# Kernel optimization log

Hardware: AMD Instinct MI355X
Metric: run time of the kernel (lower is better)

The kernel has to match this reference:

```python
import jax, jax.numpy as jnp
import numpy as np

NUM_CLASSES = 80
NMS_THRESH = 0.5      # cfg.MODEL.ROI_HEADS.NMS_THRESH_TEST
SCORE_THRESH = 0.5    # cfg.MODEL.ROI_HEADS.SCORE_THRESH_TEST
IMG_H, IMG_W = 800.0, 1333.0  # clip bounds (image_size)


def _pairwise_iou(boxes):
    # boxes: [N,4] xyxy -> IoU [N,N]
    x1, y1, x2, y2 = boxes[:, 0], boxes[:, 1], boxes[:, 2], boxes[:, 3]
    area = jnp.maximum(x2 - x1, 0.0) * jnp.maximum(y2 - y1, 0.0)
    xx1 = jnp.maximum(x1[:, None], x1[None, :])
    yy1 = jnp.maximum(y1[:, None], y1[None, :])
    xx2 = jnp.minimum(x2[:, None], x2[None, :])
    yy2 = jnp.minimum(y2[:, None], y2[None, :])
    inter = jnp.maximum(xx2 - xx1, 0.0) * jnp.maximum(yy2 - yy1, 0.0)
    union = area[:, None] + area[None, :] - inter
    return inter / jnp.maximum(union, 1e-9)


def _nms_mask(boxes, scores, thresh):
    # torchvision-style greedy NMS; returns boolean keep mask in original order
    N = boxes.shape[0]
    order = jnp.argsort(-scores)
    iou = _pairwise_iou(boxes[order])  # [N,N] in score-descending order
    idx = jnp.arange(N)

    def body(i, keep):
        # if box i survives, suppress all lower-scored boxes with IoU > thresh
        sup = (iou[i] > thresh) & keep[i] & (idx > i)
        return keep & ~sup

    keep = jax.lax.fori_loop(0, N, body, jnp.ones(N, dtype=bool))
    return jnp.zeros(N, dtype=bool).at[order].set(keep)


def setup_inputs() -> dict:
    key = jax.random.key(0)
    k1, k2, k3, k4 = jax.random.split(key, 4)
    B, N = 8, 512
    # realistic xyxy boxes inside the image
    xy = jax.random.uniform(k1, (B, N, NUM_CLASSES, 2)) * jnp.array([IMG_W, IMG_H])
    wh = jax.random.uniform(k2, (B, N, NUM_CLASSES, 2)) * 200.0 + 4.0
    boxes = jnp.concatenate([xy, xy + wh], axis=-1).astype(jnp.float32)
    score_logits = (jax.random.normal(k3, (B, N, NUM_CLASSES + 1)) * 2.0).astype(jnp.float32)
    scale = jax.random.uniform(k4, (B, 2), minval=0.5, maxval=1.5).astype(jnp.float32)
    return {"boxes": boxes, "score_logits": score_logits, "scale": scale}


def reference(boxes, score_logits, scale):
    # --- get_output_boxes: scale + clip ---
    probs = jax.nn.softmax(score_logits, axis=-1)  # [B,N,81] (predict_probs)
    s4 = jnp.stack([scale[:, 0], scale[:, 1], scale[:, 0], scale[:, 1]], axis=-1)  # [B,4]
    scaled = boxes * s4[:, None, None, :]
    hi = jnp.array([IMG_W, IMG_H, IMG_W, IMG_H], dtype=boxes.dtype)
    clipped = jnp.clip(scaled, 0.0, hi)  # [B,N,80,4]

    # --- select_boxes: per-class NMS (class-parallel instead of python loop) ---
    cls_boxes = jnp.moveaxis(clipped, 2, 1)           # [B,80,N,4]
    cls_scores = jnp.moveaxis(probs[..., 1:], 2, 1)   # [B,80,N] (skip background col 0)
    nms = jax.vmap(jax.vmap(lambda b, s: _nms_mask(b, s, NMS_THRESH)))
    keep_mask = nms(cls_boxes, cls_scores)            # [B,80,N]

    # cumulative max_conf update over classes == elementwise max over kept scores
    max_conf = jnp.max(jnp.where(keep_mask, cls_scores, 0.0), axis=1)  # [B,N]
    keep = (max_conf >= SCORE_THRESH).astype(jnp.float32)              # [B,N]
    return max_conf, keep
```

## Files before the change

kernel.cpp:

```cpp
#include <hip/hip_runtime.h>
#include <cstdint>

#define NB 8
#define NN 512
#define NC 80
#define NCL 81
#define NMS_TH 0.5f
#define SCORE_TH 0.5f
#define IMGW 1333.0f
#define IMGH 800.0f
#define CUT 0.018f

__device__ __forceinline__ uint64_t shfl_xor64(uint64_t x, int m) {
    uint32_t lo = __shfl_xor((uint32_t)(x & 0xffffffffull), m, 64);
    uint32_t hi = __shfl_xor((uint32_t)(x >> 32), m, 64);
    return ((uint64_t)hi << 32) | lo;
}
__device__ __forceinline__ float bcastf(float v, int l) {
    return __uint_as_float((uint32_t)__builtin_amdgcn_readlane((int)__float_as_uint(v), l));
}
__device__ __forceinline__ uint64_t readlane64(uint64_t v, int l) {
    uint32_t lo = (uint32_t)__builtin_amdgcn_readlane((int)(uint32_t)(v & 0xffffffffull), l);
    uint32_t hi = (uint32_t)__builtin_amdgcn_readlane((int)(uint32_t)(v >> 32), l);
    return ((uint64_t)hi << 32) | lo;
}

__global__ __launch_bounds__(256) void k_probs(const float* __restrict__ logits,
                                               float* __restrict__ probsT,
                                               float* __restrict__ maxconf,
                                               float* __restrict__ keepout) {
    __shared__ float lp[16][81];
    const int wv = threadIdx.x >> 6, lane = threadIdx.x & 63;
    const int row0 = blockIdx.x * 16;
    const int b = row0 >> 9, n0 = row0 & (NN - 1);

    for (int r = 0; r < 4; ++r) {
        const int rl = wv * 4 + r;
        const int row = row0 + rl;
        const float* p = logits + (size_t)row * NCL;
        float v0 = p[lane];
        bool has1 = (lane + 64) < NCL;
        float v1 = has1 ? p[lane + 64] : -INFINITY;
        float m = fmaxf(v0, v1);
#pragma unroll
        for (int off = 32; off; off >>= 1) m = fmaxf(m, __shfl_xor(m, off));
        float e0 = expf(v0 - m);
        float e1 = has1 ? expf(v1 - m) : 0.0f;
        float s = e0 + e1;
#pragma unroll
        for (int off = 32; off; off >>= 1) s += __shfl_xor(s, off);
        if (lane >= 1)  lp[rl][lane - 1]  = e0 / s;
        if (has1)       lp[rl][lane + 63] = e1 / s;
    }
    if (threadIdx.x < 16)                       maxconf[row0 + threadIdx.x] = 0.0f;
    else if (threadIdx.x < 32)                  keepout[row0 + (threadIdx.x - 16)] = 0.0f;
    __syncthreads();

    for (int it = 0; it < 5; ++it) {
        const int idx = it * 256 + threadIdx.x;
        const int c = idx >> 4, nl = idx & 15;
        probsT[(size_t)(b * NC + c) * NN + n0 + nl] = lp[nl][c];
    }
}

__global__ __launch_bounds__(64) void k_softmax_stats(const float* __restrict__ logits,
                                                      float* __restrict__ stats,
                                                      float* __restrict__ maxconf,
                                                      float* __restrict__ keepout) {
    int row = blockIdx.x;
    int lane = threadIdx.x;
    const float* p = logits + (size_t)row * NCL;
    float v0 = p[lane];
    bool has1 = (lane + 64) < NCL;
    float v1 = has1 ? p[lane + 64] : -INFINITY;
    float m = fmaxf(v0, v1);
#pragma unroll
    for (int off = 32; off; off >>= 1) m = fmaxf(m, __shfl_xor(m, off));
    float s = expf(v0 - m) + (has1 ? expf(v1 - m) : 0.0f);
#pragma unroll
    for (int off = 32; off; off >>= 1) s += __shfl_xor(s, off);
    if (lane == 0) { stats[2 * row] = m; stats[2 * row + 1] = s; }
    if (lane == 1) maxconf[row] = 0.0f;
    if (lane == 2) keepout[row] = 0.0f;
}

__device__ __forceinline__ void nms64(const uint64_t k0, const int M, const int lane,
                                      const float* __restrict__ boxBase,
                                      const float sx, const float sy, const int obase,
                                      float* __restrict__ maxconf,
                                      float* __restrict__ keepout) {
    float x1 = 0.f, y1 = 0.f, x2 = 0.f, y2 = 0.f, ar = 0.f;
    int nidx = 0;
    if (lane < M) {
        nidx = NN - 1 - (int)(uint32_t)(k0 & 0xffffffffull);
        const float4 bp = *reinterpret_cast<const float4*>(boxBase + (size_t)nidx * (NC * 4));
        x1 = fminf(fmaxf(bp.x * sx, 0.f), IMGW);
        y1 = fminf(fmaxf(bp.y * sy, 0.f), IMGH);
        x2 = fminf(fmaxf(bp.z * sx, 0.f), IMGW);
        y2 = fminf(fmaxf(bp.w * sy, 0.f), IMGH);
        ar = fmaxf(x2 - x1, 0.f) * fmaxf(y2 - y1, 0.f);
    }

    uint64_t pmv = 0;
    int rankv = lane;
    const int M2 = M & ~1;
    for (int ii = 0; ii < M2; ii += 2) {
        const uint64_t kA = readlane64(k0, ii);
        const uint64_t kB = readlane64(k0, ii + 1);
        const float aX1 = bcastf(x1, ii),     aY1 = bcastf(y1, ii);
        const float aX2 = bcastf(x2, ii),     aY2 = bcastf(y2, ii);
        const float aAr = bcastf(ar, ii);
        const float bX1 = bcastf(x1, ii + 1), bY1 = bcastf(y1, ii + 1);
        const float bX2 = bcastf(x2, ii + 1), bY2 = bcastf(y2, ii + 1);
        const float bAr = bcastf(ar, ii + 1);
        float dxA = fminf(aX2, x2) - fmaxf(aX1, x1);
        float dyA = fminf(aY2, y2) - fmaxf(aY1, y1);
        float dxB = fminf(bX2, x2) - fmaxf(bX1, x1);
        float dyB = fminf(bY2, y2) - fmaxf(bY1, y1);
        float inA = fmaxf(dxA, 0.f) * fmaxf(dyA, 0.f);
        float inB = fmaxf(dxB, 0.f) * fmaxf(dyB, 0.f);
        const uint64_t hibA = __ballot(k0 > kA);
        const uint64_t hibB = __ballot(k0 > kB);
        const uint64_t ioA = __ballot(inA > NMS_TH * fmaxf(aAr + ar - inA, 1e-9f));
        const uint64_t ioB = __ballot(inB > NMS_TH * fmaxf(bAr + ar - inB, 1e-9f));
        if (lane == ii)     { pmv = ioA & ~(1ull << ii);       rankv = (int)__popcll(hibA); }
        if (lane == ii + 1) { pmv = ioB & ~(1ull << (ii + 1)); rankv = (int)__popcll(hibB); }
    }
    if (M & 1) {
        const int ii = M - 1;
        const uint64_t kA = readlane64(k0, ii);
        const float aX1 = bcastf(x1, ii), aY1 = bcastf(y1, ii);
        const float aX2 = bcastf(x2, ii), aY2 = bcastf(y2, ii);
        const float aAr = bcastf(ar, ii);
        float dxA = fminf(aX2, x2) - fmaxf(aX1, x1);
        float dyA = fminf(aY2, y2) - fmaxf(aY1, y1);
        float inA = fmaxf(dxA, 0.f) * fmaxf(dyA, 0.f);
        const uint64_t hibA = __ballot(k0 > kA);
        const uint64_t ioA = __ballot(inA > NMS_TH * fmaxf(aAr + ar - inA, 1e-9f));
        if (lane == ii) { pmv = ioA & ~(1ull << ii); rankv = (int)__popcll(hibA); }
    }

    const int permv = __builtin_amdgcn_ds_permute(rankv << 2, lane);

    uint64_t rw = 0, kb = 0;
    int sNext = __builtin_amdgcn_readlane(permv, 0);
    for (int t = 0; t < M; ++t) {
        const int s = sNext;
        sNext = __builtin_amdgcn_readlane(permv, (t + 1 < M) ? (t + 1) : t);
        if (!((rw >> s) & 1ull)) {
            kb |= (1ull << s);
            rw |= readlane64(pmv, s);
        }
    }

    if (lane < M && ((kb >> lane) & 1ull)) {
        const uint32_t sb = (uint32_t)(k0 >> 32);
        atomicMax((int*)maxconf + obase + nidx, (int)sb);
        if (sb >= 0x3F000000u)
            keepout[obase + nidx] = 1.0f;
    }
}

template<int NS>
__device__ __forceinline__ void sort_desc(uint64_t (&key)[NS], const int lane) {
#pragma unroll
    for (int k = 2; k <= NS * 64; k <<= 1) {
#pragma unroll
        for (int j = k >> 1; j > 0; j >>= 1) {
            if (j >= 64) {
                const int m = j >> 6;
#pragma unroll
                for (int s = 0; s < NS; ++s) {
                    if ((s & m) == 0) {
                        const int sp = s | m;
                        const bool up = (((s << 6) & k) != 0);
                        uint64_t a = key[s], bb = key[sp];
                        bool altb = a < bb;
                        uint64_t mn = altb ? a : bb, mx = altb ? bb : a;
                        key[s]  = up ? mn : mx;
                        key[sp] = up ? mx : mn;
                    }
                }
            } else {
#pragma unroll
                for (int s = 0; s < NS; ++s) {
                    uint64_t a = key[s];
                    uint64_t bb = shfl_xor64(a, j);
                    const int v = (s << 6) | lane;
                    bool up = ((v & k) != 0);
                    bool lower = ((lane & j) == 0);
                    bool altb = a < bb;
                    uint64_t mn = altb ? a : bb, mx = altb ? bb : a;
                    key[s] = (lower == up) ? mn : mx;
                }
            }
        }
    }
}

template<int NS>
__device__ __forceinline__ void nms_core(uint64_t (&key)[NS], const int M, const int lane,
                                         const float* __restrict__ boxBase,
                                         const float sx, const float sy, const int obase,
                                         float* __restrict__ maxconf,
                                         float* __restrict__ keepout) {
    float rx1[NS], ry1[NS], rx2[NS], ry2[NS], ra[NS];
    int sidx[NS];
#pragma unroll
    for (int s = 0; s < NS; ++s) {
        rx1[s] = ry1[s] = rx2[s] = ry2[s] = ra[s] = 0.f;
        sidx[s] = 0;
        const int r = (s << 6) | lane;
        if (r < M) {
            const int n = NN - 1 - (int)(uint32_t)(key[s] & 0xffffffffull);
            sidx[s] = n;
            const float4 bp = *reinterpret_cast<const float4*>(boxBase + (size_t)n * (NC * 4));
            float x1 = fminf(fmaxf(bp.x * sx, 0.f), IMGW);
            float y1 = fminf(fmaxf(bp.y * sy, 0.f), IMGH);
            float x2 = fminf(fmaxf(bp.z * sx, 0.f), IMGW);
            float y2 = fminf(fmaxf(bp.w * sy, 0.f), IMGH);
            rx1[s] = x1; ry1[s] = y1; rx2[s] = x2; ry2[s] = y2;
            ra[s] = fmaxf(x2 - x1, 0.f) * fmaxf(y2 - y1, 0.f);
        }
    }

    uint64_t pm[NS][NS];
#pragma unroll
    for (int s = 0; s < NS; ++s)
#pragma unroll
        for (int w = 0; w < NS; ++w) pm[s][w] = 0;
#pragma unroll
    for (int s = 0; s < NS; ++s) {
        if ((s << 6) < M) {
            const int hi = min(64, M - (s << 6));
            const int hi2 = hi & ~1;
            for (int ii = 0; ii < hi2; ii += 2) {
                const float aX1 = bcastf(rx1[s], ii),     aY1 = bcastf(ry1[s], ii);
                const float aX2 = bcastf(rx2[s], ii),     aY2 = bcastf(ry2[s], ii);
                const float aAr = bcastf(ra[s],  ii);
                const float bX1 = bcastf(rx1[s], ii + 1), bY1 = bcastf(ry1[s], ii + 1);
                const float bX2 = bcastf(rx2[s], ii + 1), bY2 = bcastf(ry2[s], ii + 1);
                const float bAr = bcastf(ra[s],  ii + 1);
#pragma unroll
                for (int w = s; w < NS; ++w) {
                    if ((w << 6) < M) {
                        float dxA = fminf(aX2, rx2[w]) - fmaxf(aX1, rx1[w]);
                        float dyA = fminf(aY2, ry2[w]) - fmaxf(aY1, ry1[w]);
                        float dxB = fminf(bX2, rx2[w]) - fmaxf(bX1, rx1[w]);
                        float dyB = fminf(bY2, ry2[w]) - fmaxf(bY1, ry1[w]);
                        float inA = fmaxf(dxA, 0.f) * fmaxf(dyA, 0.f);
                        float inB = fmaxf(dxB, 0.f) * fmaxf(dyB, 0.f);
                        uint64_t bmA = __ballot(inA > NMS_TH * fmaxf(aAr + ra[w] - inA, 1e-9f));
                        uint64_t bmB = __ballot(inB > NMS_TH * fmaxf(bAr + ra[w] - inB, 1e-9f));
                        if (w == s) { bmA &= ~(1ull << ii); bmB &= ~(1ull << (ii + 1)); }
                        if (lane == ii)     pm[s][w] = bmA;
                        if (lane == ii + 1) pm[s][w] = bmB;
                    }
                }
            }
            if (hi & 1) {
                const int ii = hi - 1;
                const float aX1 = bcastf(rx1[s], ii), aY1 = bcastf(ry1[s], ii);
                const float aX2 = bcastf(rx2[s], ii), aY2 = bcastf(ry2[s], ii);
                const float aAr = bcastf(ra[s],  ii);
#pragma unroll
                for (int w = s; w < NS; ++w) {
                    if ((w << 6) < M) {
                        float dxA = fminf(aX2, rx2[w]) - fmaxf(aX1, rx1[w]);
                        float dyA = fminf(aY2, ry2[w]) - fmaxf(aY1, ry1[w]);
                        float inA = fmaxf(dxA, 0.f) * fmaxf(dyA, 0.f);
                        uint64_t bmA = __ballot(inA > NMS_TH * fmaxf(aAr + ra[w] - inA, 1e-9f));
                        if (w == s) bmA &= ~(1ull << ii);
                        if (lane == ii) pm[s][w] = bmA;
                    }
                }
            }
        }
    }

    uint64_t rw[NS], kb[NS];
#pragma unroll
    for (int s = 0; s < NS; ++s) { rw[s] = 0; kb[s] = 0; }
#pragma unroll
    for (int s = 0; s < NS; ++s) {
        if ((s << 6) < M) {
            const int Ms = M - (s << 6);
            const uint64_t valid = (Ms >= 64) ? ~0ull : ((1ull << Ms) - 1ull);
            uint64_t cand = valid & ~rw[s];
            while (cand) {
                const int l = __builtin_ctzll(cand);
                kb[s] |= (1ull << l);
#pragma unroll
                for (int w = s; w < NS; ++w)
                    if ((w << 6) < M) rw[w] |= readlane64(pm[s][w], l);
                cand = valid & ~rw[s] & ((~0ull << l) << 1);
            }
        }
    }

#pragma unroll
    for (int s = 0; s < NS; ++s) {
        const int r = (s << 6) | lane;
        if (r < M && ((kb[s] >> lane) & 1ull)) {
            const uint32_t sb = (uint32_t)(key[s] >> 32);
            atomicMax((int*)maxconf + obase + sidx[s], (int)sb);
            if (sb >= 0x3F000000u)
                keepout[obase + sidx[s]] = 1.0f;
        }
    }
}

__global__ __launch_bounds__(256) void k_nms(const float* __restrict__ boxes,
                                             const float* __restrict__ probsT,
                                             const float* __restrict__ logits,
                                             const float* __restrict__ scale,
                                             const float* __restrict__ stats,
                                             float* __restrict__ maxconf,
                                             float* __restrict__ keepout) {
    const int wv = threadIdx.x >> 6;
    const int lane = threadIdx.x & 63;
    const int prob = blockIdx.x * 4 + wv;
    const int b = prob / NC, c = prob % NC;

    __shared__ uint64_t lk[4][NN];

    uint64_t key8[8];
    int M = 0;
    if (probsT) {
        const float* pp = probsT + (size_t)(b * NC + c) * NN;
#pragma unroll
        for (int s = 0; s < 8; ++s) {
            const int n = (s << 6) | lane;
            const float p = pp[n];
            const bool pass = (p >= CUT);
            key8[s] = pass ? (((uint64_t)__float_as_uint(p) << 32) | (uint32_t)(NN - 1 - n)) : 0ull;
            M += (int)__popcll(__ballot(pass));
        }
    } else {
        const float2* st2 = (const float2*)stats;
#pragma unroll
        for (int s = 0; s < 8; ++s) {
            const int n = (s << 6) | lane;
            const int row = b * NN + n;
            float2 ms = st2[row];
            const float p = expf(logits[(size_t)row * NCL + (c + 1)] - ms.x) / ms.y;
            const bool pass = (p >= CUT);
            key8[s] = pass ? (((uint64_t)__float_as_uint(p) << 32) | (uint32_t)(NN - 1 - n)) : 0ull;
            M += (int)__popcll(__ballot(pass));
        }
    }
    if (M == 0) return;

    int cb = 0;
#pragma unroll
    for (int s = 0; s < 8; ++s) {
        const uint64_t bm = __ballot(key8[s] != 0ull);
        const int rank = cb + (int)__popcll(bm & ((1ull << lane) - 1ull));
        if (key8[s]) lk[wv][rank] = key8[s];
        cb += (int)__popcll(bm);
    }

    const float sx = scale[2 * b], sy = scale[2 * b + 1];
    const float* boxBase = boxes + (size_t)(b * NN * NC + c) * 4;
    const int obase = b * NN;

    if (M <= 64) {
        const uint64_t k0 = (lane < M) ? lk[wv][lane] : 0ull;
        nms64(k0, M, lane, boxBase, sx, sy, obase, maxconf, keepout);
    } else if (M <= 128) {
        uint64_t kk[2];
#pragma unroll
        for (int s = 0; s < 2; ++s) { const int r = (s << 6) | lane; kk[s] = (r < M) ? lk[wv][r] : 0ull; }
        sort_desc<2>(kk, lane);
        nms_core<2>(kk, M, lane, boxBase, sx, sy, obase, maxconf, keepout);
    } else if (M <= 256) {
        uint64_t kk[4];
#pragma unroll
        for (int s = 0; s < 4; ++s) { const int r = (s << 6) | lane; kk[s] = (r < M) ? lk[wv][r] : 0ull; }
        sort_desc<4>(kk, lane);
        nms_core<4>(kk, M, lane, boxBase, sx, sy, obase, maxconf, keepout);
    } else {
        uint64_t kk[8];
#pragma unroll
        for (int s = 0; s < 8; ++s) { const int r = (s << 6) | lane; kk[s] = (r < M) ? lk[wv][r] : 0ull; }
        sort_desc<8>(kk, lane);
        nms_core<8>(kk, M, lane, boxBase, sx, sy, obase, maxconf, keepout);
    }
}

extern "C" void kernel_launch(void* const* d_in, const int* in_sizes, int n_in,
                              void* d_out, int out_size, void* d_ws, size_t ws_size,
                              hipStream_t stream) {
    const float* boxes  = (const float*)d_in[0];
    const float* logits = (const float*)d_in[1];
    const float* scale  = (const float*)d_in[2];
    float* out  = (float*)d_out;
    float* keep = out + NB * NN;

    const size_t needWs = (size_t)NB * NN * NC * sizeof(float);
    if (ws_size >= needWs) {
        float* probsT = (float*)d_ws;
        hipLaunchKernelGGL(k_probs, dim3(NB * NN / 16), dim3(256), 0, stream,
                           logits, probsT, out, keep);
        hipLaunchKernelGGL(k_nms, dim3(NB * NC / 4), dim3(256), 0, stream,
                           boxes, probsT, logits, scale, (const float*)nullptr, out, keep);
    } else {
        float* stats = (float*)d_ws;
        hipLaunchKernelGGL(k_softmax_stats, dim3(NB * NN), dim3(64), 0, stream,
                           logits, stats, out, keep);
        hipLaunchKernelGGL(k_nms, dim3(NB * NC / 4), dim3(256), 0, stream,
                           boxes, (const float*)nullptr, logits, scale, stats, out, keep);
    }
}
```

Before: 28.03 us.

## Fuse softmax-transpose and NMS into one cooperative kernel with grid sync

Merges the probability/transpose kernel and the per-class NMS kernel into a single cooperative launch of 256 blocks, separated by a grid-wide barrier. Each block first computes softmax for its rows into shared memory and writes the transposed probabilities, then after the barrier its waves run NMS for their class problems, reusing the same shared buffer. This removes one kernel launch and the gap between the two kernels, at the cost of a grid sync and requiring all blocks to be co-resident. If the cooperative launch fails, it falls back to the two-kernel path.

Measured after the change: 83.77 us. 199% more time.

```diff
diff --git a/kernel.cpp b/kernel.cpp
--- a/kernel.cpp
+++ b/kernel.cpp
@@ -1,5 +1,8 @@
 #include <hip/hip_runtime.h>
+#include <hip/hip_cooperative_groups.h>
 #include <cstdint>
+
+namespace cg = cooperative_groups;
 
 #define NB 8
 #define NN 512
@@ -25,13 +28,13 @@
     return ((uint64_t)hi << 32) | lo;
 }
 
-__global__ __launch_bounds__(256) void k_probs(const float* __restrict__ logits,
-                                               float* __restrict__ probsT,
-                                               float* __restrict__ maxconf,
-                                               float* __restrict__ keepout) {
-    __shared__ float lp[16][81];
+__device__ __forceinline__ void probs16_body(const float* __restrict__ logits,
+                                             float* __restrict__ probsT,
+                                             float* __restrict__ maxconf,
+                                             float* __restrict__ keepout,
+                                             const int blk, float (*lp)[81]) {
     const int wv = threadIdx.x >> 6, lane = threadIdx.x & 63;
-    const int row0 = blockIdx.x * 16;
+    const int row0 = blk * 16;
     const int b = row0 >> 9, n0 = row0 & (NN - 1);
 
     for (int r = 0; r < 4; ++r) {
@@ -52,8 +55,8 @@
         if (lane >= 1)  lp[rl][lane - 1]  = e0 / s;
         if (has1)       lp[rl][lane + 63] = e1 / s;
     }
-    if (threadIdx.x < 16)                       maxconf[row0 + threadIdx.x] = 0.0f;
-    else if (threadIdx.x < 32)                  keepout[row0 + (threadIdx.x - 16)] = 0.0f;
+    if (threadIdx.x < 16)      maxconf[row0 + threadIdx.x] = 0.0f;
+    else if (threadIdx.x < 32) keepout[row0 + (threadIdx.x - 16)] = 0.0f;
     __syncthreads();
 
     for (int it = 0; it < 5; ++it) {
@@ -61,27 +64,6 @@
         const int c = idx >> 4, nl = idx & 15;
         probsT[(size_t)(b * NC + c) * NN + n0 + nl] = lp[nl][c];
     }
-}
-
-__global__ __launch_bounds__(64) void k_softmax_stats(const float* __restrict__ logits,
-                                                      float* __restrict__ stats,
-                                                      float* __restrict__ maxconf,
-                                                      float* __restrict__ keepout) {
-    int row = blockIdx.x;
-    int lane = threadIdx.x;
-    const float* p = logits + (size_t)row * NCL;
-    float v0 = p[lane];
-    bool has1 = (lane + 64) < NCL;
-    float v1 = has1 ? p[lane + 64] : -INFINITY;
-    float m = fmaxf(v0, v1);
-#pragma unroll
-    for (int off = 32; off; off >>= 1) m = fmaxf(m, __shfl_xor(m, off));
-    float s = expf(v0 - m) + (has1 ? expf(v1 - m) : 0.0f);
-#pragma unroll
-    for (int off = 32; off; off >>= 1) s += __shfl_xor(s, off);
-    if (lane == 0) { stats[2 * row] = m; stats[2 * row + 1] = s; }
-    if (lane == 1) maxconf[row] = 0.0f;
-    if (lane == 2) keepout[row] = 0.0f;
 }
 
 __device__ __forceinline__ void nms64(const uint64_t k0, const int M, const int lane,
@@ -310,19 +292,16 @@
     }
 }
 
-__global__ __launch_bounds__(256) void k_nms(const float* __restrict__ boxes,
-                                             const float* __restrict__ probsT,
-                                             const float* __restrict__ logits,
-                                             const float* __restrict__ scale,
-                                             const float* __restrict__ stats,
-                                             float* __restrict__ maxconf,
-                                             float* __restrict__ keepout) {
-    const int wv = threadIdx.x >> 6;
-    const int lane = threadIdx.x & 63;
-    const int prob = blockIdx.x * 4 + wv;
+__device__ __forceinline__ void nms_wave(const float* __restrict__ boxes,
+                                         const float* __restrict__ probsT,
+                                         const float* __restrict__ logits,
+                                         const float* __restrict__ scale,
+                                         const float* __restrict__ stats,
+                                         float* __restrict__ maxconf,
+                                         float* __restrict__ keepout,
+                                         const int prob, const int lane,
+                                         uint64_t* __restrict__ lkw) {
     const int b = prob / NC, c = prob % NC;
-
-    __shared__ uint64_t lk[4][NN];
 
     uint64_t key8[8];
     int M = 0;
@@ -356,7 +335,7 @@
     for (int s = 0; s < 8; ++s) {
         const uint64_t bm = __ballot(key8[s] != 0ull);
         const int rank = cb + (int)__popcll(bm & ((1ull << lane) - 1ull));
-        if (key8[s]) lk[wv][rank] = key8[s];
+        if (key8[s]) lkw[rank] = key8[s];
         cb += (int)__popcll(bm);
     }
 
@@ -365,27 +344,87 @@
     const int obase = b * NN;
 
     if (M <= 64) {
-        const uint64_t k0 = (lane < M) ? lk[wv][lane] : 0ull;
+        const uint64_t k0 = (lane < M) ? lkw[lane] : 0ull;
         nms64(k0, M, lane, boxBase, sx, sy, obase, maxconf, keepout);
     } else if (M <= 128) {
         uint64_t kk[2];
 #pragma unroll
-        for (int s = 0; s < 2; ++s) { const int r = (s << 6) | lane; kk[s] = (r < M) ? lk[wv][r] : 0ull; }
+        for (int s = 0; s < 2; ++s) { const int r = (s << 6) | lane; kk[s] = (r < M) ? lkw[r] : 0ull; }
         sort_desc<2>(kk, lane);
         nms_core<2>(kk, M, lane, boxBase, sx, sy, obase, maxconf, keepout);
     } else if (M <= 256) {
         uint64_t kk[4];
 #pragma unroll
-        for (int s = 0; s < 4; ++s) { const int r = (s << 6) | lane; kk[s] = (r < M) ? lk[wv][r] : 0ull; }
+        for (int s = 0; s < 4; ++s) { const int r = (s << 6) | lane; kk[s] = (r < M) ? lkw[r] : 0ull; }
         sort_desc<4>(kk, lane);
         nms_core<4>(kk, M, lane, boxBase, sx, sy, obase, maxconf, keepout);
     } else {
         uint64_t kk[8];
 #pragma unroll
-        for (int s = 0; s < 8; ++s) { const int r = (s << 6) | lane; kk[s] = (r < M) ? lk[wv][r] : 0ull; }
+        for (int s = 0; s < 8; ++s) { const int r = (s << 6) | lane; kk[s] = (r < M) ? lkw[r] : 0ull; }
         sort_desc<8>(kk, lane);
         nms_core<8>(kk, M, lane, boxBase, sx, sy, obase, maxconf, keepout);
     }
+}
+
+__global__ __launch_bounds__(256) void k_fused(const float* __restrict__ boxes,
+                                               const float* __restrict__ logits,
+                                               const float* __restrict__ scale,
+                                               float* __restrict__ probsT,
+                                               float* __restrict__ maxconf,
+                                               float* __restrict__ keepout) {
+    __shared__ uint64_t lk[4][NN];
+    probs16_body(logits, probsT, maxconf, keepout, blockIdx.x, (float(*)[81])lk);
+    __threadfence();
+    cg::this_grid().sync();
+
+    const int wv = threadIdx.x >> 6, lane = threadIdx.x & 63;
+    const int prob = blockIdx.x * 4 + wv;
+    if (prob >= NB * NC) return;
+    nms_wave(boxes, probsT, nullptr, scale, nullptr, maxconf, keepout, prob, lane, lk[wv]);
+}
+
+__global__ __launch_bounds__(256) void k_probs(const float* __restrict__ logits,
+                                               float* __restrict__ probsT,
+                                               float* __restrict__ maxconf,
+                                               float* __restrict__ keepout) {
+    __shared__ float lp[16][81];
+    probs16_body(logits, probsT, maxconf, keepout, blockIdx.x, lp);
+}
+
+__global__ __launch_bounds__(64) void k_softmax_stats(const float* __restrict__ logits,
+                                                      float* __restrict__ stats,
+                                                      float* __restrict__ maxconf,
+                                                      float* __restrict__ keepout) {
+    int row = blockIdx.x;
+    int lane = threadIdx.x;
+    const float* p = logits + (size_t)row * NCL;
+    float v0 = p[lane];
+    bool has1 = (lane + 64) < NCL;
+    float v1 = has1 ? p[lane + 64] : -INFINITY;
+    float m = fmaxf(v0, v1);
+#pragma unroll
+    for (int off = 32; off; off >>= 1) m = fmaxf(m, __shfl_xor(m, off));
+    float s = expf(v0 - m) + (has1 ? expf(v1 - m) : 0.0f);
+#pragma unroll
+    for (int off = 32; off; off >>= 1) s += __shfl_xor(s, off);
+    if (lane == 0) { stats[2 * row] = m; stats[2 * row + 1] = s; }
+    if (lane == 1) maxconf[row] = 0.0f;
+    if (lane == 2) keepout[row] = 0.0f;
+}
+
+__global__ __launch_bounds__(256) void k_nms(const float* __restrict__ boxes,
+                                             const float* __restrict__ probsT,
+                                             const float* __restrict__ logits,
+                                             const float* __restrict__ scale,
+                                             const float* __restrict__ stats,
+                                             float* __restrict__ maxconf,
+                                             float* __restrict__ keepout) {
+    __shared__ uint64_t lk[4][NN];
+    const int wv = threadIdx.x >> 6, lane = threadIdx.x & 63;
+    const int prob = blockIdx.x * 4 + wv;
+    if (prob >= NB * NC) return;
+    nms_wave(boxes, probsT, logits, scale, stats, maxconf, keepout, prob, lane, lk[wv]);
 }
 
 extern "C" void kernel_launch(void* const* d_in, const int* in_sizes, int n_in,
@@ -400,6 +439,12 @@
     const size_t needWs = (size_t)NB * NN * NC * sizeof(float);
     if (ws_size >= needWs) {
         float* probsT = (float*)d_ws;
+        void* args[] = {(void*)&boxes, (void*)&logits, (void*)&scale,
+                        (void*)&probsT, (void*)&out, (void*)&keep};
+        hipError_t e = hipLaunchCooperativeKernel((const void*)k_fused, dim3(256), dim3(256),
+                                                  args, 0, stream);
+        if (e == hipSuccess) return;
+        (void)hipGetLastError();
         hipLaunchKernelGGL(k_probs, dim3(NB * NN / 16), dim3(256), 0, stream,
                            logits, probsT, out, keep);
         hipLaunchKernelGGL(k_nms, dim3(NB * NC / 4), dim3(256), 0, stream,
```

## Fuse softmax statistics into NMS kernel and drop the probability workspace

Applied to the files above, without the earlier changes.

Merges the separate softmax/probability kernel and the NMS kernel into one launch. Each block recomputes the per-row softmax max and sum for all 512 rows of its batch into shared memory, then builds the per-class probabilities directly from the logits. Output initialisation is replaced by atomicMax with zero, and keep-flag writes become atomicMax, so no ordering between blocks is needed. This removes a kernel launch and the transposed probability buffer round-trip. In exchange, softmax work is repeated across the 20 blocks that share a batch, each thread reads its logits row with uncoalesced strided loads, and outputs are no longer reset to zero.

Measured after the change: 30.53 us. 1.09x slower.

```diff
diff --git a/kernel.cpp b/kernel.cpp
--- a/kernel.cpp
+++ b/kernel.cpp
@@ -23,65 +23,6 @@
     uint32_t lo = (uint32_t)__builtin_amdgcn_readlane((int)(uint32_t)(v & 0xffffffffull), l);
     uint32_t hi = (uint32_t)__builtin_amdgcn_readlane((int)(uint32_t)(v >> 32), l);
     return ((uint64_t)hi << 32) | lo;
-}
-
-__global__ __launch_bounds__(256) void k_probs(const float* __restrict__ logits,
-                                               float* __restrict__ probsT,
-                                               float* __restrict__ maxconf,
-                                               float* __restrict__ keepout) {
-    __shared__ float lp[16][81];
-    const int wv = threadIdx.x >> 6, lane = threadIdx.x & 63;
-    const int row0 = blockIdx.x * 16;
-    const int b = row0 >> 9, n0 = row0 & (NN - 1);
-
-    for (int r = 0; r < 4; ++r) {
-        const int rl = wv * 4 + r;
-        const int row = row0 + rl;
-        const float* p = logits + (size_t)row * NCL;
-        float v0 = p[lane];
-        bool has1 = (lane + 64) < NCL;
-        float v1 = has1 ? p[lane + 64] : -INFINITY;
-        float m = fmaxf(v0, v1);
-#pragma unroll
-        for (int off = 32; off; off >>= 1) m = fmaxf(m, __shfl_xor(m, off));
-        float e0 = expf(v0 - m);
-        float e1 = has1 ? expf(v1 - m) : 0.0f;
-        float s = e0 + e1;
-#pragma unroll
-        for (int off = 32; off; off >>= 1) s += __shfl_xor(s, off);
-        if (lane >= 1)  lp[rl][lane - 1]  = e0 / s;
-        if (has1)       lp[rl][lane + 63] = e1 / s;
-    }
-    if (threadIdx.x < 16)                       maxconf[row0 + threadIdx.x] = 0.0f;
-    else if (threadIdx.x < 32)                  keepout[row0 + (threadIdx.x - 16)] = 0.0f;
-    __syncthreads();
-
-    for (int it = 0; it < 5; ++it) {
-        const int idx = it * 256 + threadIdx.x;
-        const int c = idx >> 4, nl = idx & 15;
-        probsT[(size_t)(b * NC + c) * NN + n0 + nl] = lp[nl][c];
-    }
-}
-
-__global__ __launch_bounds__(64) void k_softmax_stats(const float* __restrict__ logits,
-                                                      float* __restrict__ stats,
-                                                      float* __restrict__ maxconf,
-                                                      float* __restrict__ keepout) {
-    int row = blockIdx.x;
-    int lane = threadIdx.x;
-    const float* p = logits + (size_t)row * NCL;
-    float v0 = p[lane];
-    bool has1 = (lane + 64) < NCL;
-    float v1 = has1 ? p[lane + 64] : -INFINITY;
-    float m = fmaxf(v0, v1);
-#pragma unroll
-    for (int off = 32; off; off >>= 1) m = fmaxf(m, __shfl_xor(m, off));
-    float s = expf(v0 - m) + (has1 ? expf(v1 - m) : 0.0f);
-#pragma unroll
-    for (int off = 32; off; off >>= 1) s += __shfl_xor(s, off);
-    if (lane == 0) { stats[2 * row] = m; stats[2 * row + 1] = s; }
-    if (lane == 1) maxconf[row] = 0.0f;
-    if (lane == 2) keepout[row] = 0.0f;
 }
 
 __device__ __forceinline__ void nms64(const uint64_t k0, const int M, const int lane,
@@ -157,7 +98,7 @@
         const uint32_t sb = (uint32_t)(k0 >> 32);
         atomicMax((int*)maxconf + obase + nidx, (int)sb);
         if (sb >= 0x3F000000u)
-            keepout[obase + nidx] = 1.0f;
+            atomicMax((int*)keepout + obase + nidx, 0x3F800000);
     }
 }
 
@@ -305,49 +246,68 @@
             const uint32_t sb = (uint32_t)(key[s] >> 32);
             atomicMax((int*)maxconf + obase + sidx[s], (int)sb);
             if (sb >= 0x3F000000u)
-                keepout[obase + sidx[s]] = 1.0f;
-        }
-    }
-}
-
-__global__ __launch_bounds__(256) void k_nms(const float* __restrict__ boxes,
-                                             const float* __restrict__ probsT,
+                atomicMax((int*)keepout + obase + sidx[s], 0x3F800000);
+        }
+    }
+}
+
+__global__ __launch_bounds__(256) void k_all(const float* __restrict__ boxes,
                                              const float* __restrict__ logits,
                                              const float* __restrict__ scale,
-                                             const float* __restrict__ stats,
                                              float* __restrict__ maxconf,
                                              float* __restrict__ keepout) {
-    const int wv = threadIdx.x >> 6;
-    const int lane = threadIdx.x & 63;
-    const int prob = blockIdx.x * 4 + wv;
-    const int b = prob / NC, c = prob % NC;
-
+    __shared__ float smM[NN], smS[NN];
     __shared__ uint64_t lk[4][NN];
+
+    const int wv = threadIdx.x >> 6, lane = threadIdx.x & 63;
+    const int prob0 = blockIdx.x * 4;
+    const int b = prob0 / NC;
+    const int c = (prob0 % NC) + wv;
+    const int obase = b * NN;
+
+    for (int rr = 0; rr < 2; ++rr) {
+        const int n = threadIdx.x + rr * 256;
+        const float* p = logits + (size_t)(obase + n) * NCL;
+        float a[64];
+#pragma unroll
+        for (int l = 0; l < 64; ++l) a[l] = p[l];
+        float m = a[0];
+#pragma unroll
+        for (int l = 1; l < 64; ++l) m = fmaxf(m, a[l]);
+#pragma unroll
+        for (int l = 64; l < NCL; ++l) m = fmaxf(m, p[l]);
+#pragma unroll
+        for (int l = 0; l < 64; ++l)
+            a[l] = expf(a[l] - m) + ((l + 64) < NCL ? expf(p[l + 64] - m) : 0.0f);
+#pragma unroll
+        for (int off = 32; off; off >>= 1)
+#pragma unroll
+            for (int l = 0; l < 32; ++l)
+                if (l < off) a[l] = a[l] + a[l + off];
+        smM[n] = m;
+        smS[n] = a[0];
+    }
+    __syncthreads();
+
+    if (c == 0) {
+#pragma unroll
+        for (int s = 0; s < 8; ++s) {
+            const int r = (s << 6) | lane;
+            atomicMax((int*)maxconf + obase + r, 0);
+            atomicMax((int*)keepout + obase + r, 0);
+        }
+    }
 
     uint64_t key8[8];
     int M = 0;
-    if (probsT) {
-        const float* pp = probsT + (size_t)(b * NC + c) * NN;
-#pragma unroll
-        for (int s = 0; s < 8; ++s) {
-            const int n = (s << 6) | lane;
-            const float p = pp[n];
-            const bool pass = (p >= CUT);
-            key8[s] = pass ? (((uint64_t)__float_as_uint(p) << 32) | (uint32_t)(NN - 1 - n)) : 0ull;
-            M += (int)__popcll(__ballot(pass));
-        }
-    } else {
-        const float2* st2 = (const float2*)stats;
-#pragma unroll
-        for (int s = 0; s < 8; ++s) {
-            const int n = (s << 6) | lane;
-            const int row = b * NN + n;
-            float2 ms = st2[row];
-            const float p = expf(logits[(size_t)row * NCL + (c + 1)] - ms.x) / ms.y;
-            const bool pass = (p >= CUT);
-            key8[s] = pass ? (((uint64_t)__float_as_uint(p) << 32) | (uint32_t)(NN - 1 - n)) : 0ull;
-            M += (int)__popcll(__ballot(pass));
-        }
+#pragma unroll
+    for (int s = 0; s < 8; ++s) {
+        const int n = (s << 6) | lane;
+        const float lg = logits[(size_t)(obase + n) * NCL + (c + 1)];
+        const float pr = expf(lg - smM[n]) / smS[n];
+        const bool pass = (pr >= CUT);
+        key8[s] = pass ? (((uint64_t)__float_as_uint(pr) << 32) | (uint32_t)(NN - 1 - n)) : 0ull;
+        M += (int)__popcll(__ballot(pass));
     }
     if (M == 0) return;
 
@@ -362,7 +322,6 @@
 
     const float sx = scale[2 * b], sy = scale[2 * b + 1];
     const float* boxBase = boxes + (size_t)(b * NN * NC + c) * 4;
-    const int obase = b * NN;
 
     if (M <= 64) {
         const uint64_t k0 = (lane < M) ? lk[wv][lane] : 0ull;
@@ -397,18 +356,6 @@
     float* out  = (float*)d_out;
     float* keep = out + NB * NN;
 
-    const size_t needWs = (size_t)NB * NN * NC * sizeof(float);
-    if (ws_size >= needWs) {
-        float* probsT = (float*)d_ws;
-        hipLaunchKernelGGL(k_probs, dim3(NB * NN / 16), dim3(256), 0, stream,
-                           logits, probsT, out, keep);
-        hipLaunchKernelGGL(k_nms, dim3(NB * NC / 4), dim3(256), 0, stream,
-                           boxes, probsT, logits, scale, (const float*)nullptr, out, keep);
-    } else {
-        float* stats = (float*)d_ws;
-        hipLaunchKernelGGL(k_softmax_stats, dim3(NB * NN), dim3(64), 0, stream,
-                           logits, stats, out, keep);
-        hipLaunchKernelGGL(k_nms, dim3(NB * NC / 4), dim3(256), 0, stream,
-                           boxes, (const float*)nullptr, logits, scale, stats, out, keep);
-    }
-}
+    hipLaunchKernelGGL(k_all, dim3(NB * NC / 4), dim3(256), 0, stream,
+                       boxes, logits, scale, out, keep);
+}
```
